# Optimization experiments

Measured on AMD Instinct MI355X. Metric: run time of the kernel, lower is better.

Reference implementation:

```python
import jax, jax.numpy as jnp
from jax import lax
import numpy as np

B, N, H, K = 64, 256, 1024, 3  # batch, num_proposals, hidden_dim, conv kernel size
LN_EPS = 1e-5


def setup_inputs() -> dict:
    key = jax.random.key(0)
    k1, k2, k3 = jax.random.split(key, 3)
    scale = 1.0 / np.sqrt(H)
    return {
        "f": jax.random.normal(k1, (B, N, H), dtype=jnp.float32),
        "k": jax.random.normal(k2, (B, N, H), dtype=jnp.float32),
        "W_lin": jax.random.normal(k3, (N * K, H), dtype=jnp.float32) * scale,
        "b_lin": jnp.zeros((N * K,), dtype=jnp.float32),
        "ln_gamma": jnp.ones((H,), dtype=jnp.float32),
        "ln_beta": jnp.zeros((H,), dtype=jnp.float32),
    }


def _conv_one(x, w):
    # x: [N, H] (channels, length); w: [N_out, N_in, K]
    # PyTorch F.conv1d is cross-correlation, same as lax conv with no flip.
    y = lax.conv_general_dilated(
        x[None], w, window_strides=(1,), padding="SAME",
        dimension_numbers=("NCH", "OIH", "NCH"))
    return y[0]  # [N, H]


def reference(f, k, W_lin, b_lin, ln_gamma, ln_beta):
    # Dynamic weight generation: [B, N, H] -> [B, N, N*K] -> [B, N, N, K]
    weight = jnp.einsum("bnh,oh->bno", f, W_lin) + b_lin
    weight = weight.reshape(B, N, N, K)
    # Per-sample dynamic conv1d over the hidden dim (batched via vmap)
    out = jax.vmap(_conv_one)(k, weight)  # [B, N, H]
    # LayerNorm over hidden dim
    mu = jnp.mean(out, axis=-1, keepdims=True)
    var = jnp.var(out, axis=-1, keepdims=True)
    out = (out - mu) * lax.rsqrt(var + LN_EPS) * ln_gamma + ln_beta
    return out
```

## Files before the change

### kernel.cpp

```cpp
#include <hip/hip_runtime.h>
#include <math.h>

#define Bsz 64
#define Nn  256
#define Hh  1024
#define NK  768

typedef __bf16 bf16;
typedef bf16 bf16x4 __attribute__((ext_vector_type(4)));
typedef bf16 bf16x8 __attribute__((ext_vector_type(8)));
typedef float floatx4 __attribute__((ext_vector_type(4)));

__device__ __forceinline__ void gl_lds16(const bf16* g, bf16* l) {
    __builtin_amdgcn_global_load_lds(
        (__attribute__((address_space(1))) void*)(g),
        (__attribute__((address_space(3))) void*)(l), 16, 0, 0);
}

__global__ __launch_bounds__(256) void cast2_kernel(
    const float* __restrict__ f, const float* __restrict__ wl,
    bf16* __restrict__ fbf, bf16* __restrict__ wlbf)
{
    int i = blockIdx.x * 256 + threadIdx.x;
    if (i < 4194304) {
        float4 v = ((const float4*)f)[i];
        bf16x4 o = { (bf16)v.x, (bf16)v.y, (bf16)v.z, (bf16)v.w };
        ((bf16x4*)fbf)[i] = o;
    } else {
        int j = i - 4194304;
        if (j < 196608) {
            float4 v = ((const float4*)wl)[j];
            bf16x4 o = { (bf16)v.x, (bf16)v.y, (bf16)v.z, (bf16)v.w };
            ((bf16x4*)wlbf)[j] = o;
        }
    }
}

__global__ __launch_bounds__(256) void gemm1_mfma(
    const bf16* __restrict__ A,
    const bf16* __restrict__ Bw,
    const float* __restrict__ bias,
    bf16* __restrict__ wgt3)
{
    __shared__ bf16 As[2][128 * 32];
    __shared__ bf16 Bs[2][128 * 32];
    const int tid  = threadIdx.x;
    const int wave = tid >> 6, lane = tid & 63;
    const int row0 = blockIdx.y * 128;
    const int col0 = blockIdx.x * 128;

    const bf16* gA[4]; const bf16* gB[4];
    bf16* lA[4]; bf16* lB[4];
    #pragma unroll
    for (int j = 0; j < 4; ++j) {
        int sg  = wave * 4 + j;
        int reg = sg >> 3;
        int wi  = sg & 7;
        int row = wi * 16 + (lane >> 2);
        int quad = lane & 3;
        gA[j] = A  + (size_t)(row0 + row) * Hh + reg * 32 + quad * 8;
        gB[j] = Bw + (size_t)(col0 + row) * Hh + reg * 32 + quad * 8;
        lA[j] = &As[reg][wi * 512];
        lB[j] = &Bs[reg][wi * 512];
    }

    const int wm = wave & 1, wn = wave >> 1;
    const int fm = lane & 15, koct = (lane >> 4) * 8;

    floatx4 zero = {0.f, 0.f, 0.f, 0.f};
    floatx4 acc[4][4];
    #pragma unroll
    for (int i = 0; i < 4; ++i)
        #pragma unroll
        for (int j = 0; j < 4; ++j) acc[i][j] = zero;

    for (int k0 = 0; k0 < Hh; k0 += 64) {
        #pragma unroll
        for (int j = 0; j < 4; ++j) {
            gl_lds16(gA[j] + k0, lA[j]);
            gl_lds16(gB[j] + k0, lB[j]);
        }
        __syncthreads();
        #pragma unroll
        for (int q = 0; q < 2; ++q) {
            bf16x8 af[4], bfr[4];
            #pragma unroll
            for (int mt = 0; mt < 4; ++mt)
                af[mt] = *(const bf16x8*)&As[q][(wm * 64 + mt * 16 + fm) * 32 + koct];
            #pragma unroll
            for (int nt = 0; nt < 4; ++nt)
                bfr[nt] = *(const bf16x8*)&Bs[q][(wn * 64 + nt * 16 + fm) * 32 + koct];
            #pragma unroll
            for (int mt = 0; mt < 4; ++mt)
                #pragma unroll
                for (int nt = 0; nt < 4; ++nt)
                    acc[mt][nt] = __builtin_amdgcn_mfma_f32_16x16x32_bf16(
                        af[mt], bfr[nt], acc[mt][nt], 0, 0, 0);
        }
        __syncthreads();
    }

    const int b = row0 >> 8;
    #pragma unroll
    for (int nt = 0; nt < 4; ++nt) {
        int col = col0 + wn * 64 + nt * 16 + fm;
        float bl = bias[col];
        int ii = col / 3;
        int tt = col - ii * 3;
        bf16* dst = wgt3 + ((size_t)(b * 3 + tt) << 16) + ii;
        #pragma unroll
        for (int mt = 0; mt < 4; ++mt) {
            int nr = (row0 & 255) + wm * 64 + mt * 16 + (lane >> 4) * 4;
            #pragma unroll
            for (int r = 0; r < 4; ++r)
                dst[(size_t)(nr + r) << 8] = (bf16)(acc[mt][nt][r] + bl);
        }
    }
}

__global__ __launch_bounds__(256, 2) void conv_mfma(
    const float* __restrict__ kin,
    const bf16* __restrict__ wgt3,
    float* __restrict__ out)
{
    __shared__ bf16 As[3 * 128 * 32];
    __shared__ bf16 Ks[258 * 40];
    const int tid  = threadIdx.x;
    const int wave = tid >> 6, lane = tid & 63;
    const int b  = blockIdx.z;
    const int o0 = blockIdx.y * 128;
    const int h0 = blockIdx.x * 256;
    const int wm = wave & 1, wn = wave >> 1;
    const int fm = lane & 15, koct = (lane >> 4) * 8;

    const bf16* gA[6];
    bf16* lA[6];
    #pragma unroll
    for (int j = 0; j < 6; ++j) {
        int s = (wave * 6 + j) * 64 + lane;
        int t = s >> 9, rem = s & 511;
        int o = rem >> 2, iq = rem & 3;
        gA[j] = wgt3 + ((size_t)(b * 3 + t) << 16) + ((size_t)(o0 + o) << 8) + iq * 8;
        lA[j] = &As[(wave * 6 + j) * 512];
    }
    const int ki  = tid & 31;
    const int kho = tid >> 5;
    const float* kb = kin + (size_t)b * Nn * Hh;

    floatx4 zero = {0.f, 0.f, 0.f, 0.f};
    floatx4 acc[4][8];
    #pragma unroll
    for (int i = 0; i < 4; ++i)
        #pragma unroll
        for (int j = 0; j < 8; ++j) acc[i][j] = zero;

    for (int ic = 0; ic < 8; ++ic) {
        const int i0 = ic * 32;
        __syncthreads();
        #pragma unroll
        for (int j = 0; j < 6; ++j) gl_lds16(gA[j] + i0, lA[j]);
        #pragma unroll
        for (int p = 0; p < 4; ++p) {
            int ho = kho + p * 8;
            const float* src = kb + (size_t)(i0 + ki) * Hh + h0 + ho * 8;
            float4 v0 = ((const float4*)src)[0];
            float4 v1 = ((const float4*)src)[1];
            int rb = (1 + ho * 8) * 40 + ki;
            Ks[rb + 0 * 40] = (bf16)v0.x; Ks[rb + 1 * 40] = (bf16)v0.y;
            Ks[rb + 2 * 40] = (bf16)v0.z; Ks[rb + 3 * 40] = (bf16)v0.w;
            Ks[rb + 4 * 40] = (bf16)v1.x; Ks[rb + 5 * 40] = (bf16)v1.y;
            Ks[rb + 6 * 40] = (bf16)v1.z; Ks[rb + 7 * 40] = (bf16)v1.w;
        }
        if (tid < 32) {
            Ks[tid] = (h0 > 0) ? (bf16)kb[(size_t)(i0 + tid) * Hh + h0 - 1] : (bf16)0.f;
        } else if (tid < 64) {
            int i2 = tid - 32;
            Ks[257 * 40 + i2] = (h0 + 256 < Hh)
                ? (bf16)kb[(size_t)(i0 + i2) * Hh + h0 + 256] : (bf16)0.f;
        }
        __syncthreads();
        #pragma unroll
        for (int t = 0; t < 3; ++t) {
            bf16x8 af[4], bfr[8];
            #pragma unroll
            for (int mt = 0; mt < 4; ++mt)
                af[mt] = *(const bf16x8*)&As[t * 4096 + (wm * 64 + mt * 16 + fm) * 32 + koct];
            #pragma unroll
            for (int nt = 0; nt < 8; ++nt)
                bfr[nt] = *(const bf16x8*)&Ks[(wn * 128 + nt * 16 + fm + t) * 40 + koct];
            #pragma unroll
            for (int mt = 0; mt < 4; ++mt)
                #pragma unroll
                for (int nt = 0; nt < 8; ++nt)
                    acc[mt][nt] = __builtin_amdgcn_mfma_f32_16x16x32_bf16(
                        af[mt], bfr[nt], acc[mt][nt], 0, 0, 0);
        }
    }

    #pragma unroll
    for (int mt = 0; mt < 4; ++mt) {
        int o = o0 + wm * 64 + mt * 16 + (lane >> 4) * 4;
        #pragma unroll
        for (int nt = 0; nt < 8; ++nt) {
            int h = h0 + wn * 128 + nt * 16 + fm;
            #pragma unroll
            for (int r = 0; r < 4; ++r)
                out[((size_t)(b * 256 + o + r) << 10) + h] = acc[mt][nt][r];
        }
    }
}

__global__ __launch_bounds__(256) void ln_kernel(
    float* __restrict__ io, const float* __restrict__ gamma,
    const float* __restrict__ beta)
{
    const int row = blockIdx.x;
    const int tid = threadIdx.x;
    float* p = io + ((size_t)row << 10);
    float4 v = ((const float4*)p)[tid];
    float x[4] = {v.x, v.y, v.z, v.w};
    float s1 = x[0] + x[1] + x[2] + x[3];
    float s2 = x[0]*x[0] + x[1]*x[1] + x[2]*x[2] + x[3]*x[3];
    #pragma unroll
    for (int m = 1; m < 64; m <<= 1) {
        s1 += __shfl_xor(s1, m, 64);
        s2 += __shfl_xor(s2, m, 64);
    }
    __shared__ float r1[4], r2[4];
    if ((tid & 63) == 0) { r1[tid >> 6] = s1; r2[tid >> 6] = s2; }
    __syncthreads();
    float S1 = r1[0] + r1[1] + r1[2] + r1[3];
    float S2 = r2[0] + r2[1] + r2[2] + r2[3];
    float mu   = S1 * (1.0f / 1024.0f);
    float var  = S2 * (1.0f / 1024.0f) - mu * mu;
    float rstd = rsqrtf(var + 1e-5f);
    float4 g  = ((const float4*)gamma)[tid];
    float4 be = ((const float4*)beta)[tid];
    float4 o;
    o.x = (x[0] - mu) * rstd * g.x + be.x;
    o.y = (x[1] - mu) * rstd * g.y + be.y;
    o.z = (x[2] - mu) * rstd * g.z + be.z;
    o.w = (x[3] - mu) * rstd * g.w + be.w;
    ((float4*)p)[tid] = o;
}

extern "C" void kernel_launch(void* const* d_in, const int* in_sizes, int n_in,
                              void* d_out, int out_size, void* d_ws, size_t ws_size,
                              hipStream_t stream) {
    const float* f     = (const float*)d_in[0];
    const float* kin   = (const float*)d_in[1];
    const float* W_lin = (const float*)d_in[2];
    const float* b_lin = (const float*)d_in[3];
    const float* gamma = (const float*)d_in[4];
    const float* beta  = (const float*)d_in[5];
    float* out = (float*)d_out;

    char* ws = (char*)d_ws;
    bf16* fbf  = (bf16*)(ws);
    bf16* wlbf = (bf16*)(ws + 33554432);
    bf16* wgt3 = (bf16*)(ws + 35127296);

    cast2_kernel<<<17152, 256, 0, stream>>>(f, W_lin, fbf, wlbf);
    gemm1_mfma<<<dim3(6, 128), 256, 0, stream>>>(fbf, wlbf, b_lin, wgt3);
    conv_mfma<<<dim3(4, 2, 64), 256, 0, stream>>>(kin, wgt3, out);
    ln_kernel<<<16384, 256, 0, stream>>>(out, gamma, beta);
}
```

Measured before the change: 287.3 us.

## Pre-transpose k to padded bf16 layout and coalesce gemm1 weight stores

```diff
diff --git a/kernel.cpp b/kernel.cpp
--- a/kernel.cpp
+++ b/kernel.cpp
@@ -10,6 +10,9 @@
 typedef bf16 bf16x4 __attribute__((ext_vector_type(4)));
 typedef bf16 bf16x8 __attribute__((ext_vector_type(8)));
 typedef float floatx4 __attribute__((ext_vector_type(4)));
+
+#define KT_ROWS   1026
+#define KT_BSTRIDE (KT_ROWS * 256)
 
 __device__ __forceinline__ void gl_lds16(const bf16* g, bf16* l) {
     __builtin_amdgcn_global_load_lds(
@@ -36,95 +39,141 @@
     }
 }
 
+__global__ __launch_bounds__(256) void kT_kernel(
+    const float* __restrict__ kin, bf16* __restrict__ kTp)
+{
+    __shared__ bf16 T[64 * 72];
+    const int tid = threadIdx.x;
+    const int b = blockIdx.z, i0 = blockIdx.y * 64, h0 = blockIdx.x * 64;
+    const float* src = kin + ((size_t)b << 18);
+    bf16* dstb = kTp + (size_t)b * KT_BSTRIDE;
+
+    if (blockIdx.x == 0 && blockIdx.y == 0) {
+        dstb[tid] = (bf16)0.f;
+        dstb[(size_t)1025 * 256 + tid] = (bf16)0.f;
+    }
+    #pragma unroll
+    for (int j = 0; j < 4; ++j) {
+        int s = tid + j * 256;
+        int il = s >> 4, c4 = s & 15;
+        float4 v = *(const float4*)&src[(size_t)(i0 + il) * Hh + h0 + c4 * 4];
+        T[(c4 * 4 + 0) * 72 + il] = (bf16)v.x;
+        T[(c4 * 4 + 1) * 72 + il] = (bf16)v.y;
+        T[(c4 * 4 + 2) * 72 + il] = (bf16)v.z;
+        T[(c4 * 4 + 3) * 72 + il] = (bf16)v.w;
+    }
+    __syncthreads();
+    #pragma unroll
+    for (int p = 0; p < 2; ++p) {
+        int hl = (tid >> 3) + p * 32;
+        int q  = tid & 7;
+        bf16x8 v = *(const bf16x8*)&T[hl * 72 + q * 8];
+        *(bf16x8*)&dstb[(size_t)(h0 + hl + 1) * 256 + i0 + q * 8] = v;
+    }
+}
+
 __global__ __launch_bounds__(256) void gemm1_mfma(
     const bf16* __restrict__ A,
     const bf16* __restrict__ Bw,
     const float* __restrict__ bias,
     bf16* __restrict__ wgt3)
 {
-    __shared__ bf16 As[2][128 * 32];
-    __shared__ bf16 Bs[2][128 * 32];
+    __shared__ bf16 smem[14336];
+    bf16* As = smem;
+    bf16* Bs = smem + 8192;
     const int tid  = threadIdx.x;
     const int wave = tid >> 6, lane = tid & 63;
     const int row0 = blockIdx.y * 128;
-    const int col0 = blockIdx.x * 128;
-
-    const bf16* gA[4]; const bf16* gB[4];
-    bf16* lA[4]; bf16* lB[4];
+    const int col0 = blockIdx.x * 96;
+
+    const bf16* gA[4]; bf16* lA[4];
     #pragma unroll
     for (int j = 0; j < 4; ++j) {
-        int sg  = wave * 4 + j;
-        int reg = sg >> 3;
-        int wi  = sg & 7;
-        int row = wi * 16 + (lane >> 2);
-        int quad = lane & 3;
-        gA[j] = A  + (size_t)(row0 + row) * Hh + reg * 32 + quad * 8;
+        int s = tid + j * 256;
+        int reg = s >> 9, rem = s & 511, row = rem >> 2, quad = rem & 3;
+        gA[j] = A + (size_t)(row0 + row) * Hh + reg * 32 + quad * 8;
+        lA[j] = As + s * 8;
+    }
+    const bf16* gB[3]; bf16* lB[3];
+    #pragma unroll
+    for (int j = 0; j < 3; ++j) {
+        int s = tid + j * 256;
+        int reg = s / 384, rem = s - reg * 384, row = rem >> 2, quad = rem & 3;
         gB[j] = Bw + (size_t)(col0 + row) * Hh + reg * 32 + quad * 8;
-        lA[j] = &As[reg][wi * 512];
-        lB[j] = &Bs[reg][wi * 512];
+        lB[j] = Bs + s * 8;
     }
 
     const int wm = wave & 1, wn = wave >> 1;
     const int fm = lane & 15, koct = (lane >> 4) * 8;
 
     floatx4 zero = {0.f, 0.f, 0.f, 0.f};
-    floatx4 acc[4][4];
+    floatx4 acc[4][3];
     #pragma unroll
     for (int i = 0; i < 4; ++i)
         #pragma unroll
-        for (int j = 0; j < 4; ++j) acc[i][j] = zero;
+        for (int j = 0; j < 3; ++j) acc[i][j] = zero;
 
     for (int k0 = 0; k0 < Hh; k0 += 64) {
         #pragma unroll
-        for (int j = 0; j < 4; ++j) {
-            gl_lds16(gA[j] + k0, lA[j]);
-            gl_lds16(gB[j] + k0, lB[j]);
-        }
+        for (int j = 0; j < 4; ++j) gl_lds16(gA[j] + k0, lA[j]);
+        #pragma unroll
+        for (int j = 0; j < 3; ++j) gl_lds16(gB[j] + k0, lB[j]);
         __syncthreads();
         #pragma unroll
         for (int q = 0; q < 2; ++q) {
-            bf16x8 af[4], bfr[4];
+            bf16x8 af[4], bfr[3];
             #pragma unroll
             for (int mt = 0; mt < 4; ++mt)
-                af[mt] = *(const bf16x8*)&As[q][(wm * 64 + mt * 16 + fm) * 32 + koct];
-            #pragma unroll
-            for (int nt = 0; nt < 4; ++nt)
-                bfr[nt] = *(const bf16x8*)&Bs[q][(wn * 64 + nt * 16 + fm) * 32 + koct];
+                af[mt] = *(const bf16x8*)&As[q * 4096 + (wm * 64 + mt * 16 + fm) * 32 + koct];
+            #pragma unroll
+            for (int nt = 0; nt < 3; ++nt)
+                bfr[nt] = *(const bf16x8*)&Bs[q * 3072 + (wn * 48 + nt * 16 + fm) * 32 + koct];
             #pragma unroll
             for (int mt = 0; mt < 4; ++mt)
                 #pragma unroll
-                for (int nt = 0; nt < 4; ++nt)
+                for (int nt = 0; nt < 3; ++nt)
                     acc[mt][nt] = __builtin_amdgcn_mfma_f32_16x16x32_bf16(
                         af[mt], bfr[nt], acc[mt][nt], 0, 0, 0);
         }
         __syncthreads();
     }
 
-    const int b = row0 >> 8;
-    #pragma unroll
-    for (int nt = 0; nt < 4; ++nt) {
-        int col = col0 + wn * 64 + nt * 16 + fm;
-        float bl = bias[col];
-        int ii = col / 3;
-        int tt = col - ii * 3;
-        bf16* dst = wgt3 + ((size_t)(b * 3 + tt) << 16) + ii;
+    const int b  = row0 >> 8;
+    const int nb = row0 & 255;
+    bf16* Cs = smem;
+    #pragma unroll
+    for (int nt = 0; nt < 3; ++nt) {
+        int c = wn * 48 + nt * 16 + fm;
+        float bl = bias[col0 + c];
         #pragma unroll
         for (int mt = 0; mt < 4; ++mt) {
-            int nr = (row0 & 255) + wm * 64 + mt * 16 + (lane >> 4) * 4;
+            int rb = wm * 64 + mt * 16 + (lane >> 4) * 4;
             #pragma unroll
             for (int r = 0; r < 4; ++r)
-                dst[(size_t)(nr + r) << 8] = (bf16)(acc[mt][nt][r] + bl);
-        }
+                Cs[(rb + r) * 104 + c] = (bf16)(acc[mt][nt][r] + bl);
+        }
+    }
+    __syncthreads();
+    const int i0 = blockIdx.x * 32;
+    #pragma unroll
+    for (int j = 0; j < 6; ++j) {
+        int s = tid + j * 256;
+        int t = s / 512, rem = s & 511, n = rem >> 2, q8 = rem & 3;
+        bf16x8 v;
+        #pragma unroll
+        for (int u = 0; u < 8; ++u)
+            v[u] = Cs[n * 104 + (q8 * 8 + u) * 3 + t];
+        *(bf16x8*)&wgt3[((size_t)(b * 3 + t) << 16) + ((size_t)(nb + n) << 8) + i0 + q8 * 8] = v;
     }
 }
 
 __global__ __launch_bounds__(256, 2) void conv_mfma(
-    const float* __restrict__ kin,
+    const bf16* __restrict__ kTp,
     const bf16* __restrict__ wgt3,
     float* __restrict__ out)
 {
-    __shared__ bf16 As[3 * 128 * 32];
-    __shared__ bf16 Ks[258 * 40];
+    __shared__ bf16 As[12288];
+    __shared__ bf16 Ks[8704];
     const int tid  = threadIdx.x;
     const int wave = tid >> 6, lane = tid & 63;
     const int b  = blockIdx.z;
@@ -133,19 +182,23 @@
     const int wm = wave & 1, wn = wave >> 1;
     const int fm = lane & 15, koct = (lane >> 4) * 8;
 
-    const bf16* gA[6];
-    bf16* lA[6];
+    const bf16* gA[6]; bf16* lA[6];
     #pragma unroll
     for (int j = 0; j < 6; ++j) {
-        int s = (wave * 6 + j) * 64 + lane;
-        int t = s >> 9, rem = s & 511;
-        int o = rem >> 2, iq = rem & 3;
+        int s = tid + j * 256;
+        int t = s / 512, rem = s & 511, o = rem >> 2, iq = rem & 3;
         gA[j] = wgt3 + ((size_t)(b * 3 + t) << 16) + ((size_t)(o0 + o) << 8) + iq * 8;
-        lA[j] = &As[(wave * 6 + j) * 512];
-    }
-    const int ki  = tid & 31;
-    const int kho = tid >> 5;
-    const float* kb = kin + (size_t)b * Nn * Hh;
+        lA[j] = As + s * 8;
+    }
+    const bf16* kb = kTp + (size_t)b * KT_BSTRIDE;
+    const bf16* gK[4]; bf16* lK[4];
+    #pragma unroll
+    for (int j = 0; j < 4; ++j) {
+        int s = tid + j * 256;
+        int r = s >> 2, quad = s & 3;
+        gK[j] = kb + (size_t)(h0 + r) * 256 + quad * 8;
+        lK[j] = Ks + s * 8;
+    }
 
     floatx4 zero = {0.f, 0.f, 0.f, 0.f};
     floatx4 acc[4][8];
@@ -160,23 +213,11 @@
         #pragma unroll
         for (int j = 0; j < 6; ++j) gl_lds16(gA[j] + i0, lA[j]);
         #pragma unroll
-        for (int p = 0; p < 4; ++p) {
-            int ho = kho + p * 8;
-            const float* src = kb + (size_t)(i0 + ki) * Hh + h0 + ho * 8;
-            float4 v0 = ((const float4*)src)[0];
-            float4 v1 = ((const float4*)src)[1];
-            int rb = (1 + ho * 8) * 40 + ki;
-            Ks[rb + 0 * 40] = (bf16)v0.x; Ks[rb + 1 * 40] = (bf16)v0.y;
-            Ks[rb + 2 * 40] = (bf16)v0.z; Ks[rb + 3 * 40] = (bf16)v0.w;
-            Ks[rb + 4 * 40] = (bf16)v1.x; Ks[rb + 5 * 40] = (bf16)v1.y;
-            Ks[rb + 6 * 40] = (bf16)v1.z; Ks[rb + 7 * 40] = (bf16)v1.w;
-        }
-        if (tid < 32) {
-            Ks[tid] = (h0 > 0) ? (bf16)kb[(size_t)(i0 + tid) * Hh + h0 - 1] : (bf16)0.f;
-        } else if (tid < 64) {
-            int i2 = tid - 32;
-            Ks[257 * 40 + i2] = (h0 + 256 < Hh)
-                ? (bf16)kb[(size_t)(i0 + i2) * Hh + h0 + 256] : (bf16)0.f;
+        for (int j = 0; j < 4; ++j) gl_lds16(gK[j] + i0, lK[j]);
+        if (tid < 8) {
+            int r = 256 + (tid >> 2), q = tid & 3;
+            bf16x8 v = *(const bf16x8*)&kb[(size_t)(h0 + r) * 256 + i0 + q * 8];
+            *(bf16x8*)&Ks[r * 32 + q * 8] = v;
         }
         __syncthreads();
         #pragma unroll
@@ -187,7 +228,7 @@
                 af[mt] = *(const bf16x8*)&As[t * 4096 + (wm * 64 + mt * 16 + fm) * 32 + koct];
             #pragma unroll
             for (int nt = 0; nt < 8; ++nt)
-                bfr[nt] = *(const bf16x8*)&Ks[(wn * 128 + nt * 16 + fm + t) * 40 + koct];
+                bfr[nt] = *(const bf16x8*)&Ks[(wn * 128 + nt * 16 + fm + t) * 32 + koct];
             #pragma unroll
             for (int mt = 0; mt < 4; ++mt)
                 #pragma unroll
@@ -257,11 +298,13 @@
 
     char* ws = (char*)d_ws;
     bf16* fbf  = (bf16*)(ws);
-    bf16* wlbf = (bf16*)(ws + 33554432);
-    bf16* wgt3 = (bf16*)(ws + 35127296);
+    bf16* kTp  = (bf16*)(ws);
+    bf16* wlbf = (bf16*)(ws + 33619968);
+    bf16* wgt3 = (bf16*)(ws + 35192832);
 
     cast2_kernel<<<17152, 256, 0, stream>>>(f, W_lin, fbf, wlbf);
-    gemm1_mfma<<<dim3(6, 128), 256, 0, stream>>>(fbf, wlbf, b_lin, wgt3);
-    conv_mfma<<<dim3(4, 2, 64), 256, 0, stream>>>(kin, wgt3, out);
+    gemm1_mfma<<<dim3(8, 128), 256, 0, stream>>>(fbf, wlbf, b_lin, wgt3);
+    kT_kernel<<<dim3(16, 4, 64), 256, 0, stream>>>(kin, kTp);
+    conv_mfma<<<dim3(4, 2, 64), 256, 0, stream>>>(kTp, wgt3, out);
     ln_kernel<<<16384, 256, 0, stream>>>(out, gamma, beta);
 }
```

Measured after the change: 287.0 us. About the same (-0.1%).
